# Kernel optimization log

Hardware: AMD Instinct MI355X
Metric: run time of the kernel (lower is better)

Reference implementation:

```python
import jax, jax.numpy as jnp
import numpy as np

N_E = 8192
E_DIM = 256
BETA = 0.25
ORTHO_COEF = 1.0


def setup_inputs() -> dict:
    key = jax.random.key(0)
    k1, k2 = jax.random.split(key)
    z = jax.random.normal(k1, (16, E_DIM, 32, 32), dtype=jnp.float32)
    # nn.Embedding init: uniform(-1/n_e, 1/n_e)
    codebook = jax.random.uniform(k2, (N_E, E_DIM), dtype=jnp.float32,
                                  minval=-1.0 / N_E, maxval=1.0 / N_E)
    return {"z": z, "codebook": codebook}


def reference(z, codebook):
    B, C, H, W = z.shape
    n_e = codebook.shape[0]
    zt = jnp.transpose(z, (0, 2, 3, 1))            # (B,H,W,C)
    zf = zt.reshape(-1, C)                          # (N,C)

    # L2 distances: ||z||^2 + ||e||^2 - 2 z.e
    d = (jnp.sum(zf * zf, axis=1, keepdims=True)
         + jnp.sum(codebook * codebook, axis=1)
         - 2.0 * jnp.matmul(zf, codebook.T))        # (N, n_e)
    idx = jnp.argmin(d, axis=1)                     # (N,)

    z_q_flat = codebook[idx]                        # gather == one-hot @ codebook
    z_q = z_q_flat.reshape(zt.shape)                # (B,H,W,C)

    sg = jax.lax.stop_gradient
    loss = (BETA * jnp.mean((sg(z_q) - zt) ** 2)
            + jnp.mean((z_q - sg(zt)) ** 2))

    # ortho regularizer (force_emb_len_1 == False branch)
    wn = codebook / jnp.linalg.norm(codebook, axis=1, keepdims=True)
    diff = jnp.matmul(wn, wn.T) - jnp.eye(n_e, dtype=codebook.dtype)
    ortho_reg_term = ORTHO_COEF * jnp.sum(diff ** 2) / (n_e ** 2)

    # straight-through estimator
    z_q_st = zt + sg(z_q - zt)

    # perplexity from mean one-hot usage
    N = zf.shape[0]
    counts = jnp.zeros((n_e,), dtype=zt.dtype).at[idx].add(1.0)
    e_mean = counts / N
    perplexity = jnp.exp(-jnp.sum(e_mean * jnp.log(e_mean + 1e-10)))

    z_q_out = jnp.transpose(z_q_st, (0, 3, 1, 2))   # (B,C,H,W)
    return z_q_out, loss, ortho_reg_term, perplexity, idx
```

## Files before the change

kernel.cpp:

```cpp
#include <hip/hip_runtime.h>
#include <hip/hip_bf16.h>
#include <math.h>


#define N_E     8192
#define C_DIM   256
#define N_VEC   16384
#define N_ELEM  4194304
#define MARGIN  6.0e-4f

#define WS_COUNTS   0
#define WS_M        32768
#define WS_ACCUM    294912
#define WS_LISTLEN  294944
#define WS_ZERO_BYTES 295200
#define WS_CE       295200
#define WS_RN       327968
#define WS_A        360736
#define WS_KEYS     426272
#define WS_LISTS    557344
#define WS_TILEMIN  4751648
#define WS_ZBF      8945952
#define WS_CBBF     17334560
#define WS_ZT       21528864

typedef short short8v __attribute__((ext_vector_type(8)));
typedef float f32x4  __attribute__((ext_vector_type(4)));

__device__ inline unsigned short f2bf(float f) {
    unsigned int x = __float_as_uint(f);
    return (unsigned short)((x + 0x7fffu + ((x >> 16) & 1u)) >> 16);
}

__device__ inline void gload16(const void* g, void* l) {
    __builtin_amdgcn_global_load_lds(
        (const __attribute__((address_space(1))) unsigned int*)g,
        (__attribute__((address_space(3))) unsigned int*)l, 16, 0, 0);
}

__global__ __launch_bounds__(256) void k_cbprep(const float* __restrict__ cb,
                                                float* __restrict__ ce,
                                                float* __restrict__ rn,
                                                unsigned short* __restrict__ cbbf) {
    int j = blockIdx.x;
    int tid = threadIdx.x;
    float v = cb[(size_t)j * C_DIM + tid];
    cbbf[(size_t)j * C_DIM + tid] = f2bf(v);
    float s = v * v;
    #pragma unroll
    for (int off = 32; off > 0; off >>= 1) s += __shfl_down(s, off, 64);
    __shared__ float sh[4];
    if ((tid & 63) == 0) sh[tid >> 6] = s;
    __syncthreads();
    if (tid == 0) {
        float t = sh[0] + sh[1] + sh[2] + sh[3];
        ce[j] = t;
        rn[j] = 1.0f / sqrtf(t);
    }
}

__global__ __launch_bounds__(256) void k_ztrans(const float* __restrict__ z,
                                                unsigned short* __restrict__ zbf,
                                                float* __restrict__ zT,
                                                float* __restrict__ A) {
    __shared__ float tile[64 * 260];
    const int tid = threadIdx.x;
    const int n0 = blockIdx.x * 64;
    const int b = n0 >> 10, hw0 = n0 & 1023;
    const float* zp = z + (size_t)b * 262144 + hw0;

    const int hw = tid & 63, cg = tid >> 6;
    #pragma unroll 8
    for (int p = 0; p < 64; ++p) {
        int c = p * 4 + cg;
        tile[hw * 260 + c] = zp[(size_t)c * 1024 + hw];
    }
    __syncthreads();

    if (tid < 64) {
        float a = 0.0f;
        #pragma unroll 8
        for (int c = 0; c < C_DIM; ++c) {
            float v = tile[tid * 260 + c];
            a = fmaf(v, v, a);
        }
        A[n0 + tid] = a;
    }

    const int r = tid >> 2, q = tid & 3;
    unsigned short* dst = zbf + (size_t)(n0 + r) * C_DIM + q * 64;
    float* dstT         = zT  + (size_t)(n0 + r) * C_DIM + q * 64;
    const float* src = &tile[r * 260 + q * 64];
    #pragma unroll
    for (int i = 0; i < 8; ++i) {
        f32x4 lo = *(const f32x4*)&src[i * 8];
        f32x4 hi = *(const f32x4*)&src[i * 8 + 4];
        *(f32x4*)&dstT[i * 8]     = lo;
        *(f32x4*)&dstT[i * 8 + 4] = hi;
        short8v u;
        #pragma unroll
        for (int x = 0; x < 4; ++x) { u[x] = (short)f2bf(lo[x]); u[4 + x] = (short)f2bf(hi[x]); }
        *(short8v*)(dst + i * 8) = u;
    }
}

__global__ __launch_bounds__(256) void k_mfma(const unsigned short* __restrict__ zbf,
                                              const unsigned short* __restrict__ cbbf,
                                              float* __restrict__ tilemin) {
    __shared__ unsigned short As[128 * 64];
    __shared__ unsigned short Bs[128 * 64];
    __shared__ float smin[128][2];

    const int tid = threadIdx.x;
    const int lin = blockIdx.x;
    const int x = lin & 7, r = lin >> 3;
    const int jp = r >> 7, q = r & 127;
    const int by = x * 16 + (q >> 3), bx = jp * 8 + (q & 7);
    const int n0 = by * 128, j0 = bx * 128;
    const int wave = tid >> 6, lane = tid & 63;
    const int wx = wave & 1, wy = wave >> 1;
    const int g = lane >> 4, c = lane & 15;

    const int lrow  = lane >> 3;
    const int lslot = (lane & 7) ^ lrow;
    const int rbase = wave * 32;

    f32x4 acc[4][4];
    #pragma unroll
    for (int i = 0; i < 4; ++i)
        #pragma unroll
        for (int j = 0; j < 4; ++j) acc[i][j] = (f32x4){0.f, 0.f, 0.f, 0.f};

    for (int kc = 0; kc < C_DIM; kc += 64) {
        __syncthreads();
        #pragma unroll
        for (int i = 0; i < 4; ++i) {
            const int row8 = rbase + i * 8;
            const unsigned short* ga =
                zbf  + (size_t)(n0 + row8 + lrow) * C_DIM + kc + lslot * 8;
            const unsigned short* gb =
                cbbf + (size_t)(j0 + row8 + lrow) * C_DIM + kc + lslot * 8;
            gload16(ga, &As[row8 * 64]);
            gload16(gb, &Bs[row8 * 64]);
        }
        __syncthreads();

        #pragma unroll
        for (int kk = 0; kk < 2; ++kk) {
            short8v a[4], b[4];
            #pragma unroll
            for (int f = 0; f < 4; ++f) {
                const int row = wy * 64 + f * 16 + c;
                a[f] = *(const short8v*)&As[row * 64 + (((kk * 4 + g) ^ (c & 7)) * 8)];
            }
            #pragma unroll
            for (int f = 0; f < 4; ++f) {
                const int row = wx * 64 + f * 16 + c;
                b[f] = *(const short8v*)&Bs[row * 64 + (((kk * 4 + g) ^ (c & 7)) * 8)];
            }
            #pragma unroll
            for (int nf = 0; nf < 4; ++nf)
                #pragma unroll
                for (int jf = 0; jf < 4; ++jf)
                    acc[nf][jf] = __builtin_amdgcn_mfma_f32_16x16x32_bf16(
                        a[nf], b[jf], acc[nf][jf], 0, 0, 0);
        }
    }

    #pragma unroll
    for (int nf = 0; nf < 4; ++nf) {
        #pragma unroll
        for (int rr = 0; rr < 4; ++rr) {
            float mx = acc[nf][0][rr];
            #pragma unroll
            for (int jf = 1; jf < 4; ++jf) mx = fmaxf(mx, acc[nf][jf][rr]);
            #pragma unroll
            for (int off = 1; off < 16; off <<= 1)
                mx = fmaxf(mx, __shfl_xor(mx, off, 64));
            if (c == 0) smin[wy * 64 + nf * 16 + g * 4 + rr][wx] = -2.0f * mx;
        }
    }
    __syncthreads();
    if (tid < 128)
        tilemin[(size_t)bx * N_VEC + n0 + tid] = fminf(smin[tid][0], smin[tid][1]);
}

__global__ __launch_bounds__(256) void k_cand2(const float* __restrict__ tilemin,
                                               unsigned long long* __restrict__ keys,
                                               int* __restrict__ listlen,
                                               int* __restrict__ lists) {
    __shared__ float red[4][64];
    __shared__ float thr_s[64];
    const int nl = threadIdx.x & 63, tg = threadIdx.x >> 6;
    const int n = blockIdx.x * 64 + nl;

    float m = 3.4e38f;
    #pragma unroll
    for (int i = 0; i < 16; ++i)
        m = fminf(m, tilemin[(size_t)(tg * 16 + i) * N_VEC + n]);
    red[tg][nl] = m;
    __syncthreads();
    if (tg == 0) {
        thr_s[nl] = fminf(fminf(red[0][nl], red[1][nl]),
                          fminf(red[2][nl], red[3][nl])) + MARGIN;
        keys[n] = ~0ull;
    }
    __syncthreads();
    const float thr = thr_s[nl];

    #pragma unroll
    for (int i = 0; i < 16; ++i) {
        const int t = tg * 16 + i;
        bool qq = tilemin[(size_t)t * N_VEC + n] <= thr;
        unsigned long long mask = __ballot(qq);
        if (mask) {
            int ldr = __ffsll(mask) - 1;
            int base = 0;
            if (nl == ldr) base = atomicAdd(&listlen[t], __popcll(mask));
            base = __shfl(base, ldr, 64);
            if (qq) {
                int pre = __popcll(mask & ((1ull << nl) - 1ull));
                lists[t * N_VEC + base + pre] = n;
            }
        }
    }
}

__global__ __launch_bounds__(256) void k_refine2(const float* __restrict__ zT,
                                                 const float* __restrict__ cb,
                                                 const float* __restrict__ ce,
                                                 const float* __restrict__ A,
                                                 const int* __restrict__ listlen,
                                                 const int* __restrict__ lists,
                                                 unsigned long long* __restrict__ keys) {
    __shared__ float e_s[128 * 68];
    __shared__ float z_s[32 * 68];
    __shared__ int   rows_s[32];

    const int t = blockIdx.x;
    const int len = listlen[t];
    const int tid = threadIdx.x;
    const int jg = tid & 31, rg = tid >> 5;
    const int j0 = t * 128;

    for (int b0 = blockIdx.y * 32; b0 < len; b0 += 128 * 32) {
        const int nrows = min(32, len - b0);
        __syncthreads();
        if (tid < 32)
            rows_s[tid] = lists[t * N_VEC + b0 + min(tid, nrows - 1)];

        float acc[4][4];
        #pragma unroll
        for (int rr = 0; rr < 4; ++rr)
            #pragma unroll
            for (int jj = 0; jj < 4; ++jj) acc[rr][jj] = 0.0f;

        for (int kc = 0; kc < C_DIM; kc += 64) {
            __syncthreads();
            {
                int jr = tid >> 1, ko = (tid & 1) * 32;
                #pragma unroll
                for (int i = 0; i < 8; ++i)
                    *(float4*)&e_s[jr * 68 + ko + i * 4] =
                        *(const float4*)&cb[(size_t)(j0 + jr) * C_DIM + kc + ko + i * 4];
            }
            {
                int r = tid >> 3, ko = (tid & 7) * 8;
                const float* zp = &zT[(size_t)rows_s[r] * C_DIM + kc + ko];
                *(float4*)&z_s[r * 68 + ko]     = *(const float4*)&zp[0];
                *(float4*)&z_s[r * 68 + ko + 4] = *(const float4*)&zp[4];
            }
            __syncthreads();

            #pragma unroll
            for (int k4 = 0; k4 < 16; ++k4) {
                float4 ef[4], zf[4];
                #pragma unroll
                for (int jj = 0; jj < 4; ++jj)
                    ef[jj] = *(const float4*)&e_s[(jg + 32 * jj) * 68 + k4 * 4];
                #pragma unroll
                for (int rr = 0; rr < 4; ++rr)
                    zf[rr] = *(const float4*)&z_s[(rg * 4 + rr) * 68 + k4 * 4];
                #pragma unroll
                for (int kk = 0; kk < 4; ++kk)
                    #pragma unroll
                    for (int rr = 0; rr < 4; ++rr)
                        #pragma unroll
                        for (int jj = 0; jj < 4; ++jj)
                            acc[rr][jj] = fmaf(((const float*)&zf[rr])[kk],
                                               ((const float*)&ef[jj])[kk], acc[rr][jj]);
            }
        }

        #pragma unroll
        for (int rr = 0; rr < 4; ++rr) {
            const int n = rows_s[rg * 4 + rr];
            const float An = A[n];
            unsigned long long best = ~0ull;
            #pragma unroll
            for (int jj = 0; jj < 4; ++jj) {
                int j = j0 + jg + 32 * jj;
                float tt = An + ce[j];
                float d = fmaf(-2.0f, acc[rr][jj], tt);
                unsigned int sd = __float_as_uint(d);
                sd = (sd & 0x80000000u) ? ~sd : (sd | 0x80000000u);
                unsigned long long key = ((unsigned long long)sd << 32) | (unsigned)j;
                best = key < best ? key : best;
            }
            #pragma unroll
            for (int off = 16; off > 0; off >>= 1) {
                unsigned long long o = __shfl_xor(best, off, 64);
                best = o < best ? o : best;
            }
            if (jg == 0) atomicMin(&keys[n], best);
        }
    }
}

__global__ __launch_bounds__(256) void k_gather(const float* __restrict__ z,
                                                const float* __restrict__ cb,
                                                const unsigned long long* __restrict__ keys,
                                                float* __restrict__ out,
                                                float* __restrict__ out_idx,
                                                int* __restrict__ counts,
                                                double* __restrict__ sse) {
    int bh = blockIdx.x;
    int b = bh >> 5, h = bh & 31;
    int tid = threadIdx.x;
    __shared__ int sidx[32];
    if (tid < 32) {
        int n = b * 1024 + h * 32 + tid;
        unsigned long long k = keys[n];
        int idx = (int)(k & 0xFFFFFFFFull);
        sidx[tid] = idx;
        out_idx[n] = (float)idx;
        atomicAdd(&counts[idx], 1);
    }
    __syncthreads();
    int w = tid & 31, cy = tid >> 5;
    int jid = sidx[w];
    const float* cbr = cb + (size_t)jid * C_DIM;
    size_t zb = (size_t)b * 262144 + h * 32 + w;

    double acc = 0.0;
    #pragma unroll 4
    for (int cc = 0; cc < 32; ++cc) {
        int c = cc * 8 + cy;
        float e = cbr[c];
        size_t zi = zb + (size_t)c * 1024;
        float d = e - z[zi];
        out[zi] = e;
        acc += (double)(d * d);
    }
    #pragma unroll
    for (int off = 32; off > 0; off >>= 1) acc += __shfl_down(acc, off, 64);
    __shared__ double sh[4];
    if ((tid & 63) == 0) sh[tid >> 6] = acc;
    __syncthreads();
    if (tid == 0) atomicAdd(sse, sh[0] + sh[1] + sh[2] + sh[3]);
}

__global__ __launch_bounds__(256) void k_gram(const float* __restrict__ cb,
                                              const float* __restrict__ rn,
                                              float* __restrict__ M) {
    __shared__ float aT[64][68];
    __shared__ float bT[64][68];
    int k0 = blockIdx.x * 64, l0 = blockIdx.y * 64;
    int jc0 = blockIdx.z * 256;
    int tid = threadIdx.x;
    int tk = tid & 15, tl = tid >> 4;
    float acc[4][4];
    #pragma unroll
    for (int i = 0; i < 4; ++i)
        #pragma unroll
        for (int l = 0; l < 4; ++l) acc[i][l] = 0.0f;

    for (int jc = jc0; jc < jc0 + 256; jc += 64) {
        __syncthreads();
        {
            int kk = tid & 63, jj0 = tid >> 6;
            #pragma unroll
            for (int p = 0; p < 16; ++p) {
                int jj = p * 4 + jj0;
                float r = rn[jc + jj];
                const float* row = cb + (size_t)(jc + jj) * C_DIM;
                aT[jj][kk] = row[k0 + kk] * r;
                bT[jj][kk] = row[l0 + kk] * r;
            }
        }
        __syncthreads();
        #pragma unroll 8
        for (int jj = 0; jj < 64; ++jj) {
            float4 av = *(const float4*)&aT[jj][tk * 4];
            float4 bv = *(const float4*)&bT[jj][tl * 4];
            float a4[4] = {av.x, av.y, av.z, av.w};
            float b4[4] = {bv.x, bv.y, bv.z, bv.w};
            #pragma unroll
            for (int i = 0; i < 4; ++i)
                #pragma unroll
                for (int l = 0; l < 4; ++l)
                    acc[i][l] = fmaf(a4[i], b4[l], acc[i][l]);
        }
    }
    #pragma unroll
    for (int i = 0; i < 4; ++i)
        #pragma unroll
        for (int l = 0; l < 4; ++l)
            atomicAdd(&M[(size_t)(k0 + tk * 4 + i) * C_DIM + l0 + tl * 4 + l], acc[i][l]);
}

__global__ __launch_bounds__(256) void k_msq(const float* __restrict__ M,
                                             const int* __restrict__ counts,
                                             double* __restrict__ accum) {
    const int tid = threadIdx.x, bid = blockIdx.x;
    __shared__ double sh[4];
    double s = 0.0;
    if (bid < 64) {
        const float* p = &M[bid * 1024 + tid * 4];
        float4 v = *(const float4*)p;
        s = (double)v.x * v.x + (double)v.y * v.y
          + (double)v.z * v.z + (double)v.w * v.w;
    } else {
        int j = (bid - 64) * 256 + tid;
        double p = counts[j] * (1.0 / (double)N_VEC);
        s = p * log(p + 1e-10);
    }
    #pragma unroll
    for (int off = 32; off > 0; off >>= 1) s += __shfl_down(s, off, 64);
    if ((tid & 63) == 0) sh[tid >> 6] = s;
    __syncthreads();
    if (tid == 0)
        atomicAdd(&accum[bid < 64 ? 1 : 2], sh[0] + sh[1] + sh[2] + sh[3]);
}

__global__ __launch_bounds__(64) void k_final(const double* __restrict__ accum,
                                              float* __restrict__ out_scalars) {
    if (threadIdx.x == 0) {
        out_scalars[0] = (float)(1.25 * accum[0] / (double)N_ELEM);
        out_scalars[1] = (float)((accum[1] - (double)N_E) / ((double)N_E * N_E));
        out_scalars[2] = (float)exp(-accum[2]);
    }
}

extern "C" void kernel_launch(void* const* d_in, const int* in_sizes, int n_in,
                              void* d_out, int out_size, void* d_ws, size_t ws_size,
                              hipStream_t stream) {
    (void)in_sizes; (void)n_in; (void)out_size; (void)ws_size;
    const float* z  = (const float*)d_in[0];
    const float* cb = (const float*)d_in[1];
    float* out = (float*)d_out;

    char* ws = (char*)d_ws;
    int* counts            = (int*)(ws + WS_COUNTS);
    float* M               = (float*)(ws + WS_M);
    double* accum          = (double*)(ws + WS_ACCUM);
    int* listlen           = (int*)(ws + WS_LISTLEN);
    float* ce              = (float*)(ws + WS_CE);
    float* rn              = (float*)(ws + WS_RN);
    float* A               = (float*)(ws + WS_A);
    unsigned long long* keys = (unsigned long long*)(ws + WS_KEYS);
    int* lists             = (int*)(ws + WS_LISTS);
    float* tilemin         = (float*)(ws + WS_TILEMIN);
    unsigned short* zbf    = (unsigned short*)(ws + WS_ZBF);
    unsigned short* cbbf   = (unsigned short*)(ws + WS_CBBF);
    float* zT              = (float*)(ws + WS_ZT);

    float* out_scalars = out + N_ELEM;
    float* out_idx     = out + N_ELEM + 3;

    hipMemsetAsync(ws, 0, WS_ZERO_BYTES, stream);

    k_cbprep<<<N_E, 256, 0, stream>>>(cb, ce, rn, cbbf);
    k_ztrans<<<N_VEC / 64, 256, 0, stream>>>(z, zbf, zT, A);
    k_mfma<<<8192, 256, 0, stream>>>(zbf, cbbf, tilemin);
    k_cand2<<<N_VEC / 64, 256, 0, stream>>>(tilemin, keys, listlen, lists);
    k_refine2<<<dim3(64, 128), 256, 0, stream>>>(zT, cb, ce, A, listlen, lists, keys);
    k_gather<<<512, 256, 0, stream>>>(z, cb, keys, out, out_idx, counts, accum);
    k_gram<<<dim3(4, 4, 32), 256, 0, stream>>>(cb, rn, M);
    k_msq<<<96, 256, 0, stream>>>(M, counts, accum);
    k_final<<<1, 64, 0, stream>>>(accum, out_scalars);
}
```

Before: 343.1 us.

## Merge prep, candidate/gram, gather/msq kernels and drop the workspace memset

Horizontally fuses independent kernels by giving each its own block range: codebook prep plus z transpose (which now also zeroes the counters, M and accumulators in place of the memset), candidate selection plus the gram matrix, and the gather plus the M sum-of-squares. The perplexity entropy moves into a single-block final kernel. This cuts the launch count from nine operations to five and lets the gram work run alongside candidate selection. The cost is more shared memory per fused block, and correctness now depends on the zeroing finishing before later kernels use those buffers, which stream order provides.

```diff
diff --git a/kernel.cpp b/kernel.cpp
--- a/kernel.cpp
+++ b/kernel.cpp
@@ -13,7 +13,6 @@
 #define WS_M        32768
 #define WS_ACCUM    294912
 #define WS_LISTLEN  294944
-#define WS_ZERO_BYTES 295200
 #define WS_CE       295200
 #define WS_RN       327968
 #define WS_A        360736
@@ -38,69 +37,83 @@
         (__attribute__((address_space(3))) unsigned int*)l, 16, 0, 0);
 }
 
-__global__ __launch_bounds__(256) void k_cbprep(const float* __restrict__ cb,
-                                                float* __restrict__ ce,
-                                                float* __restrict__ rn,
-                                                unsigned short* __restrict__ cbbf) {
-    int j = blockIdx.x;
-    int tid = threadIdx.x;
-    float v = cb[(size_t)j * C_DIM + tid];
-    cbbf[(size_t)j * C_DIM + tid] = f2bf(v);
-    float s = v * v;
-    #pragma unroll
-    for (int off = 32; off > 0; off >>= 1) s += __shfl_down(s, off, 64);
-    __shared__ float sh[4];
-    if ((tid & 63) == 0) sh[tid >> 6] = s;
-    __syncthreads();
-    if (tid == 0) {
-        float t = sh[0] + sh[1] + sh[2] + sh[3];
-        ce[j] = t;
-        rn[j] = 1.0f / sqrtf(t);
-    }
-}
-
-__global__ __launch_bounds__(256) void k_ztrans(const float* __restrict__ z,
-                                                unsigned short* __restrict__ zbf,
-                                                float* __restrict__ zT,
-                                                float* __restrict__ A) {
+__global__ __launch_bounds__(256) void k_prep(const float* __restrict__ cb,
+                                              const float* __restrict__ z,
+                                              float* __restrict__ ce,
+                                              float* __restrict__ rn,
+                                              unsigned short* __restrict__ cbbf,
+                                              unsigned short* __restrict__ zbf,
+                                              float* __restrict__ zT,
+                                              float* __restrict__ A,
+                                              float* __restrict__ M,
+                                              int* __restrict__ counts,
+                                              int* __restrict__ listlen,
+                                              double* __restrict__ accum) {
     __shared__ float tile[64 * 260];
     const int tid = threadIdx.x;
-    const int n0 = blockIdx.x * 64;
-    const int b = n0 >> 10, hw0 = n0 & 1023;
-    const float* zp = z + (size_t)b * 262144 + hw0;
-
-    const int hw = tid & 63, cg = tid >> 6;
-    #pragma unroll 8
-    for (int p = 0; p < 64; ++p) {
-        int c = p * 4 + cg;
-        tile[hw * 260 + c] = zp[(size_t)c * 1024 + hw];
-    }
-    __syncthreads();
-
-    if (tid < 64) {
-        float a = 0.0f;
+
+    if (blockIdx.x < 8192) {
+        const int j = blockIdx.x;
+        if (tid == 0) {
+            counts[j] = 0;
+            if (j < 64) listlen[j] = 0;
+            if (j == 0) {
+                accum[0] = 0.0; accum[1] = 0.0; accum[2] = 0.0; accum[3] = 0.0;
+            }
+        }
+        float v = cb[(size_t)j * C_DIM + tid];
+        cbbf[(size_t)j * C_DIM + tid] = f2bf(v);
+        float s = v * v;
+        #pragma unroll
+        for (int off = 32; off > 0; off >>= 1) s += __shfl_down(s, off, 64);
+        if ((tid & 63) == 0) tile[tid >> 6] = s;
+        __syncthreads();
+        if (tid == 0) {
+            float t = tile[0] + tile[1] + tile[2] + tile[3];
+            ce[j] = t;
+            rn[j] = 1.0f / sqrtf(t);
+        }
+    } else {
+        const int bz = blockIdx.x - 8192;
+        M[bz * 256 + tid] = 0.0f;
+
+        const int n0 = bz * 64;
+        const int b = n0 >> 10, hw0 = n0 & 1023;
+        const float* zp = z + (size_t)b * 262144 + hw0;
+
+        const int hw = tid & 63, cg = tid >> 6;
         #pragma unroll 8
-        for (int c = 0; c < C_DIM; ++c) {
-            float v = tile[tid * 260 + c];
-            a = fmaf(v, v, a);
-        }
-        A[n0 + tid] = a;
-    }
-
-    const int r = tid >> 2, q = tid & 3;
-    unsigned short* dst = zbf + (size_t)(n0 + r) * C_DIM + q * 64;
-    float* dstT         = zT  + (size_t)(n0 + r) * C_DIM + q * 64;
-    const float* src = &tile[r * 260 + q * 64];
-    #pragma unroll
-    for (int i = 0; i < 8; ++i) {
-        f32x4 lo = *(const f32x4*)&src[i * 8];
-        f32x4 hi = *(const f32x4*)&src[i * 8 + 4];
-        *(f32x4*)&dstT[i * 8]     = lo;
-        *(f32x4*)&dstT[i * 8 + 4] = hi;
-        short8v u;
-        #pragma unroll
-        for (int x = 0; x < 4; ++x) { u[x] = (short)f2bf(lo[x]); u[4 + x] = (short)f2bf(hi[x]); }
-        *(short8v*)(dst + i * 8) = u;
+        for (int p = 0; p < 64; ++p) {
+            int c = p * 4 + cg;
+            tile[hw * 260 + c] = zp[(size_t)c * 1024 + hw];
+        }
+        __syncthreads();
+
+        if (tid < 64) {
+            float a = 0.0f;
+            #pragma unroll 8
+            for (int c = 0; c < C_DIM; ++c) {
+                float v = tile[tid * 260 + c];
+                a = fmaf(v, v, a);
+            }
+            A[n0 + tid] = a;
+        }
+
+        const int r = tid >> 2, q = tid & 3;
+        unsigned short* dst = zbf + (size_t)(n0 + r) * C_DIM + q * 64;
+        float* dstT         = zT  + (size_t)(n0 + r) * C_DIM + q * 64;
+        const float* src = &tile[r * 260 + q * 64];
+        #pragma unroll
+        for (int i = 0; i < 8; ++i) {
+            f32x4 lo = *(const f32x4*)&src[i * 8];
+            f32x4 hi = *(const f32x4*)&src[i * 8 + 4];
+            *(f32x4*)&dstT[i * 8]     = lo;
+            *(f32x4*)&dstT[i * 8 + 4] = hi;
+            short8v u;
+            #pragma unroll
+            for (int x = 0; x < 4; ++x) { u[x] = (short)f2bf(lo[x]); u[4 + x] = (short)f2bf(hi[x]); }
+            *(short8v*)(dst + i * 8) = u;
+        }
     }
 }
 
@@ -185,44 +198,97 @@
         tilemin[(size_t)bx * N_VEC + n0 + tid] = fminf(smin[tid][0], smin[tid][1]);
 }
 
-__global__ __launch_bounds__(256) void k_cand2(const float* __restrict__ tilemin,
-                                               unsigned long long* __restrict__ keys,
-                                               int* __restrict__ listlen,
-                                               int* __restrict__ lists) {
-    __shared__ float red[4][64];
-    __shared__ float thr_s[64];
-    const int nl = threadIdx.x & 63, tg = threadIdx.x >> 6;
-    const int n = blockIdx.x * 64 + nl;
-
-    float m = 3.4e38f;
-    #pragma unroll
-    for (int i = 0; i < 16; ++i)
-        m = fminf(m, tilemin[(size_t)(tg * 16 + i) * N_VEC + n]);
-    red[tg][nl] = m;
-    __syncthreads();
-    if (tg == 0) {
-        thr_s[nl] = fminf(fminf(red[0][nl], red[1][nl]),
-                          fminf(red[2][nl], red[3][nl])) + MARGIN;
-        keys[n] = ~0ull;
-    }
-    __syncthreads();
-    const float thr = thr_s[nl];
-
-    #pragma unroll
-    for (int i = 0; i < 16; ++i) {
-        const int t = tg * 16 + i;
-        bool qq = tilemin[(size_t)t * N_VEC + n] <= thr;
-        unsigned long long mask = __ballot(qq);
-        if (mask) {
-            int ldr = __ffsll(mask) - 1;
-            int base = 0;
-            if (nl == ldr) base = atomicAdd(&listlen[t], __popcll(mask));
-            base = __shfl(base, ldr, 64);
-            if (qq) {
-                int pre = __popcll(mask & ((1ull << nl) - 1ull));
-                lists[t * N_VEC + base + pre] = n;
-            }
-        }
+__global__ __launch_bounds__(256) void k_candgram(const float* __restrict__ tilemin,
+                                                  unsigned long long* __restrict__ keys,
+                                                  int* __restrict__ listlen,
+                                                  int* __restrict__ lists,
+                                                  const float* __restrict__ cb,
+                                                  const float* __restrict__ rn,
+                                                  float* __restrict__ M) {
+    __shared__ float buf[2 * 64 * 68];
+    const int tid = threadIdx.x;
+
+    if (blockIdx.x < 256) {
+        float* red   = buf;
+        float* thr_s = buf + 256;
+        const int nl = tid & 63, tg = tid >> 6;
+        const int n = blockIdx.x * 64 + nl;
+
+        float m = 3.4e38f;
+        #pragma unroll
+        for (int i = 0; i < 16; ++i)
+            m = fminf(m, tilemin[(size_t)(tg * 16 + i) * N_VEC + n]);
+        red[tg * 64 + nl] = m;
+        __syncthreads();
+        if (tg == 0) {
+            thr_s[nl] = fminf(fminf(red[0 * 64 + nl], red[1 * 64 + nl]),
+                              fminf(red[2 * 64 + nl], red[3 * 64 + nl])) + MARGIN;
+            keys[n] = ~0ull;
+        }
+        __syncthreads();
+        const float thr = thr_s[nl];
+
+        #pragma unroll
+        for (int i = 0; i < 16; ++i) {
+            const int t = tg * 16 + i;
+            bool qq = tilemin[(size_t)t * N_VEC + n] <= thr;
+            unsigned long long mask = __ballot(qq);
+            if (mask) {
+                int ldr = __ffsll(mask) - 1;
+                int base = 0;
+                if (nl == ldr) base = atomicAdd(&listlen[t], __popcll(mask));
+                base = __shfl(base, ldr, 64);
+                if (qq) {
+                    int pre = __popcll(mask & ((1ull << nl) - 1ull));
+                    lists[t * N_VEC + base + pre] = n;
+                }
+            }
+        }
+    } else {
+        float* aT = buf;
+        float* bT = buf + 64 * 68;
+        const int gidx = blockIdx.x - 256;
+        const int k0 = (gidx & 3) * 64, l0 = ((gidx >> 2) & 3) * 64;
+        const int jc0 = (gidx >> 4) * 256;
+        const int tk = tid & 15, tl = tid >> 4;
+        float acc[4][4];
+        #pragma unroll
+        for (int i = 0; i < 4; ++i)
+            #pragma unroll
+            for (int l = 0; l < 4; ++l) acc[i][l] = 0.0f;
+
+        for (int jc = jc0; jc < jc0 + 256; jc += 64) {
+            __syncthreads();
+            {
+                int kk = tid & 63, jj0 = tid >> 6;
+                #pragma unroll
+                for (int p = 0; p < 16; ++p) {
+                    int jj = p * 4 + jj0;
+                    float rr = rn[jc + jj];
+                    const float* row = cb + (size_t)(jc + jj) * C_DIM;
+                    aT[jj * 68 + kk] = row[k0 + kk] * rr;
+                    bT[jj * 68 + kk] = row[l0 + kk] * rr;
+                }
+            }
+            __syncthreads();
+            #pragma unroll 8
+            for (int jj = 0; jj < 64; ++jj) {
+                float4 av = *(const float4*)&aT[jj * 68 + tk * 4];
+                float4 bv = *(const float4*)&bT[jj * 68 + tl * 4];
+                float a4[4] = {av.x, av.y, av.z, av.w};
+                float b4[4] = {bv.x, bv.y, bv.z, bv.w};
+                #pragma unroll
+                for (int i = 0; i < 4; ++i)
+                    #pragma unroll
+                    for (int l = 0; l < 4; ++l)
+                        acc[i][l] = fmaf(a4[i], b4[l], acc[i][l]);
+            }
+        }
+        #pragma unroll
+        for (int i = 0; i < 4; ++i)
+            #pragma unroll
+            for (int l = 0; l < 4; ++l)
+                atomicAdd(&M[(size_t)(k0 + tk * 4 + i) * C_DIM + l0 + tl * 4 + l], acc[i][l]);
     }
 }
 
@@ -320,14 +386,30 @@
 __global__ __launch_bounds__(256) void k_gather(const float* __restrict__ z,
                                                 const float* __restrict__ cb,
                                                 const unsigned long long* __restrict__ keys,
+                                                const float* __restrict__ M,
                                                 float* __restrict__ out,
                                                 float* __restrict__ out_idx,
                                                 int* __restrict__ counts,
-                                                double* __restrict__ sse) {
+                                                double* __restrict__ accum) {
+    const int tid = threadIdx.x;
+    __shared__ int sidx[32];
+    __shared__ double sh[4];
+
+    if (blockIdx.x >= 512) {
+        const int bid = blockIdx.x - 512;
+        float4 v = *(const float4*)&M[bid * 1024 + tid * 4];
+        double s = (double)v.x * v.x + (double)v.y * v.y
+                 + (double)v.z * v.z + (double)v.w * v.w;
+        #pragma unroll
+        for (int off = 32; off > 0; off >>= 1) s += __shfl_down(s, off, 64);
+        if ((tid & 63) == 0) sh[tid >> 6] = s;
+        __syncthreads();
+        if (tid == 0) atomicAdd(&accum[1], sh[0] + sh[1] + sh[2] + sh[3]);
+        return;
+    }
+
     int bh = blockIdx.x;
     int b = bh >> 5, h = bh & 31;
-    int tid = threadIdx.x;
-    __shared__ int sidx[32];
     if (tid < 32) {
         int n = b * 1024 + h * 32 + tid;
         unsigned long long k = keys[n];
@@ -354,91 +436,30 @@
     }
     #pragma unroll
     for (int off = 32; off > 0; off >>= 1) acc += __shfl_down(acc, off, 64);
-    __shared__ double sh[4];
     if ((tid & 63) == 0) sh[tid >> 6] = acc;
     __syncthreads();
-    if (tid == 0) atomicAdd(sse, sh[0] + sh[1] + sh[2] + sh[3]);
-}
-
-__global__ __launch_bounds__(256) void k_gram(const float* __restrict__ cb,
-                                              const float* __restrict__ rn,
-                                              float* __restrict__ M) {
-    __shared__ float aT[64][68];
-    __shared__ float bT[64][68];
-    int k0 = blockIdx.x * 64, l0 = blockIdx.y * 64;
-    int jc0 = blockIdx.z * 256;
-    int tid = threadIdx.x;
-    int tk = tid & 15, tl = tid >> 4;
-    float acc[4][4];
+    if (tid == 0) atomicAdd(&accum[0], sh[0] + sh[1] + sh[2] + sh[3]);
+}
+
+__global__ __launch_bounds__(256) void k_final(const int* __restrict__ counts,
+                                               const double* __restrict__ accum,
+                                               float* __restrict__ out_scalars) {
+    const int tid = threadIdx.x;
+    __shared__ double sh[4];
+    double h = 0.0;
+    for (int j = tid; j < N_E; j += 256) {
+        double p = counts[j] * (1.0 / (double)N_VEC);
+        h += p * log(p + 1e-10);
+    }
     #pragma unroll
-    for (int i = 0; i < 4; ++i)
-        #pragma unroll
-        for (int l = 0; l < 4; ++l) acc[i][l] = 0.0f;
-
-    for (int jc = jc0; jc < jc0 + 256; jc += 64) {
-        __syncthreads();
-        {
-            int kk = tid & 63, jj0 = tid >> 6;
-            #pragma unroll
-            for (int p = 0; p < 16; ++p) {
-                int jj = p * 4 + jj0;
-                float r = rn[jc + jj];
-                const float* row = cb + (size_t)(jc + jj) * C_DIM;
-                aT[jj][kk] = row[k0 + kk] * r;
-                bT[jj][kk] = row[l0 + kk] * r;
-            }
-        }
-        __syncthreads();
-        #pragma unroll 8
-        for (int jj = 0; jj < 64; ++jj) {
-            float4 av = *(const float4*)&aT[jj][tk * 4];
-            float4 bv = *(const float4*)&bT[jj][tl * 4];
-            float a4[4] = {av.x, av.y, av.z, av.w};
-            float b4[4] = {bv.x, bv.y, bv.z, bv.w};
-            #pragma unroll
-            for (int i = 0; i < 4; ++i)
-                #pragma unroll
-                for (int l = 0; l < 4; ++l)
-                    acc[i][l] = fmaf(a4[i], b4[l], acc[i][l]);
-        }
-    }
-    #pragma unroll
-    for (int i = 0; i < 4; ++i)
-        #pragma unroll
-        for (int l = 0; l < 4; ++l)
-            atomicAdd(&M[(size_t)(k0 + tk * 4 + i) * C_DIM + l0 + tl * 4 + l], acc[i][l]);
-}
-
-__global__ __launch_bounds__(256) void k_msq(const float* __restrict__ M,
-                                             const int* __restrict__ counts,
-                                             double* __restrict__ accum) {
-    const int tid = threadIdx.x, bid = blockIdx.x;
-    __shared__ double sh[4];
-    double s = 0.0;
-    if (bid < 64) {
-        const float* p = &M[bid * 1024 + tid * 4];
-        float4 v = *(const float4*)p;
-        s = (double)v.x * v.x + (double)v.y * v.y
-          + (double)v.z * v.z + (double)v.w * v.w;
-    } else {
-        int j = (bid - 64) * 256 + tid;
-        double p = counts[j] * (1.0 / (double)N_VEC);
-        s = p * log(p + 1e-10);
-    }
-    #pragma unroll
-    for (int off = 32; off > 0; off >>= 1) s += __shfl_down(s, off, 64);
-    if ((tid & 63) == 0) sh[tid >> 6] = s;
+    for (int off = 32; off > 0; off >>= 1) h += __shfl_down(h, off, 64);
+    if ((tid & 63) == 0) sh[tid >> 6] = h;
     __syncthreads();
-    if (tid == 0)
-        atomicAdd(&accum[bid < 64 ? 1 : 2], sh[0] + sh[1] + sh[2] + sh[3]);
-}
-
-__global__ __launch_bounds__(64) void k_final(const double* __restrict__ accum,
-                                              float* __restrict__ out_scalars) {
-    if (threadIdx.x == 0) {
+    if (tid == 0) {
+        double H = sh[0] + sh[1] + sh[2] + sh[3];
         out_scalars[0] = (float)(1.25 * accum[0] / (double)N_ELEM);
         out_scalars[1] = (float)((accum[1] - (double)N_E) / ((double)N_E * N_E));
-        out_scalars[2] = (float)exp(-accum[2]);
+        out_scalars[2] = (float)exp(-H);
     }
 }
 
@@ -468,15 +489,11 @@
     float* out_scalars = out + N_ELEM;
     float* out_idx     = out + N_ELEM + 3;
 
-    hipMemsetAsync(ws, 0, WS_ZERO_BYTES, stream);
-
-    k_cbprep<<<N_E, 256, 0, stream>>>(cb, ce, rn, cbbf);
-    k_ztrans<<<N_VEC / 64, 256, 0, stream>>>(z, zbf, zT, A);
+    k_prep<<<8448, 256, 0, stream>>>(cb, z, ce, rn, cbbf, zbf, zT, A,
+                                     M, counts, listlen, accum);
     k_mfma<<<8192, 256, 0, stream>>>(zbf, cbbf, tilemin);
-    k_cand2<<<N_VEC / 64, 256, 0, stream>>>(tilemin, keys, listlen, lists);
+    k_candgram<<<768, 256, 0, stream>>>(tilemin, keys, listlen, lists, cb, rn, M);
     k_refine2<<<dim3(64, 128), 256, 0, stream>>>(zT, cb, ce, A, listlen, lists, keys);
-    k_gather<<<512, 256, 0, stream>>>(z, cb, keys, out, out_idx, counts, accum);
-    k_gram<<<dim3(4, 4, 32), 256, 0, stream>>>(cb, rn, M);
-    k_msq<<<96, 256, 0, stream>>>(M, counts, accum);
-    k_final<<<1, 64, 0, stream>>>(accum, out_scalars);
-}
+    k_gather<<<576, 256, 0, stream>>>(z, cb, keys, M, out, out_idx, counts, accum);
+    k_final<<<1, 256, 0, stream>>>(counts, accum, out_scalars);
+}
```

Result: no change. 341.8 us (-0.4%).
